# Kernel optimization log

Hardware: AMD Instinct MI355X
Metric: run time of the kernel (lower is better)

Reference implementation:

```python
import jax, jax.numpy as jnp
import numpy as np
import itertools

DIM, ORDER = 8, 4  # matches init_kwargs

def _exponent_table(dim, order):
    # All multisets (non-decreasing tuples) of size 0..order over range(dim),
    # sorted lexicographically -- identical to sorted(Counter keys) in the torch code
    # (Counter keys are sorted tuples; combinations_with_replacement yields exactly those).
    terms = sorted(itertools.chain.from_iterable(
        itertools.combinations_with_replacement(range(dim), o) for o in range(order + 1)))
    E = np.zeros((len(terms), dim), dtype=np.int32)
    for i, t in enumerate(terms):
        for d in t:
            E[i, d] += 1
    return E

E = jnp.asarray(_exponent_table(DIM, ORDER))  # [nterms=495, dim=8]


def setup_inputs() -> dict:
    key = jax.random.key(0)
    x = jax.random.normal(key, (65536, DIM), dtype=jnp.float32)
    return {"x": x}


def reference(x):
    # torch: cat_i prod_d x[..., d] ** ind_i.count(d)
    # vectorized: broadcast pow with exponent table, reduce-product over dim axis
    # x: [B, dim] -> [B, 1, dim] ** [nterms, dim] -> prod over dim -> [B, nterms]
    return jnp.prod(x[..., None, :] ** E, axis=-1)
```

## Files before the change

kernel.cpp:

```cpp
#include <hip/hip_runtime.h>


typedef float f32x4 __attribute__((ext_vector_type(4)));

struct Tbl {
    unsigned short e[64][8][4];
    unsigned short pp[64];
};

constexpr int pidx_c(int a, int b) {
    return 9 + 8 * a - (a * (a - 1)) / 2 + (b - a);
}

constexpr Tbl make_tbl() {
    Tbl T{};
    unsigned short lin[512] = {};
    int idx = 1;
    for (int a = 0; a < 8; ++a) {
        lin[idx++] = (unsigned short)(1 + a);
        for (int b = a; b < 8; ++b) {
            lin[idx++] = (unsigned short)pidx_c(a, b);
            for (int c = b; c < 8; ++c) {
                lin[idx++] = (unsigned short)(pidx_c(a, b) | ((1 + c) << 8));
                for (int d = c; d < 8; ++d)
                    lin[idx++] = (unsigned short)(pidx_c(a, b) | (pidx_c(c, d) << 8));
            }
        }
    }
    for (int l = 0; l < 64; ++l)
        for (int c = 0; c < 8; ++c)
            for (int k = 0; k < 4; ++k) {
                int ei = c * 256 + 4 * l + k;
                if (ei < 1980) {
                    int r = ei / 495, t = ei % 495;
                    int u = lin[t] & 255, v = lin[t] >> 8;
                    T.e[l][c][k] = (unsigned short)((r * 64 + u) | ((r * 64 + v) << 8));
                } else {
                    T.e[l][c][k] = 0;
                }
            }
    for (int l = 0; l < 64; ++l) {
        int s1 = 0, s2 = 0, u1 = 0, u2 = 0;
        if (l >= 1 && l <= 8) { s1 = l - 1; u1 = 1; }
        else if (l >= 9 && l < 45) {
            int k = l - 9, i = 0;
            while (k >= 8 - i) { k -= 8 - i; ++i; }
            s1 = i; s2 = i + k; u1 = 1; u2 = 1;
        }
        T.pp[l] = (unsigned short)(s1 | (s2 << 4) | (u1 << 8) | (u2 << 9));
    }
    return T;
}

__constant__ Tbl TBL = make_tbl();

#define WAVES_PER_BLOCK 4
#define ROWS_PER_WAVE   8
#define ROWS_PER_BLOCK  (WAVES_PER_BLOCK * ROWS_PER_WAVE)

__global__ __launch_bounds__(256, 8) void TotalDegree_29755533426739_kernel(
    const float* __restrict__ x, float* __restrict__ out, int B) {
    __shared__ float xs[ROWS_PER_BLOCK * 8];
    __shared__ float Pl[WAVES_PER_BLOCK][256];

    const int tid  = (int)threadIdx.x;
    const int lane = tid & 63;
    const int wid  = tid >> 6;

    {
        const int gi = (int)blockIdx.x * (ROWS_PER_BLOCK * 8) + tid;
        xs[tid] = (gi < B * 8) ? x[gi] : 0.0f;
    }

    const int ppv  = (int)TBL.pp[lane];
    const int s1   = ppv & 15;
    const int s2   = (ppv >> 4) & 15;
    const bool use1 = ((ppv >> 8) & 1) != 0;
    const bool use2 = ((ppv >> 9) & 1) != 0;

    unsigned long long tw[8];
    #pragma unroll
    for (int c = 0; c < 8; ++c)
        tw[c] = *reinterpret_cast<const unsigned long long*>(&TBL.e[lane][c][0]);

    __syncthreads();

    const float* xw = xs + wid * (ROWS_PER_WAVE * 8);
    float* Pw = Pl[wid];
    const unsigned rowBase =
        (unsigned)blockIdx.x * ROWS_PER_BLOCK + (unsigned)(wid * ROWS_PER_WAVE);

    #pragma unroll
    for (int g = 0; g < 2; ++g) {
        #pragma unroll
        for (int r = 0; r < 4; ++r) {
            const float a1 = xw[(g * 4 + r) * 8 + s1];
            const float a2 = xw[(g * 4 + r) * 8 + s2];
            Pw[r * 64 + lane] = (use1 ? a1 : 1.0f) * (use2 ? a2 : 1.0f);
        }

        float* o = out + (rowBase + (unsigned)(g * 4)) * 495u;
        f32x4* ob = reinterpret_cast<f32x4*>(o) + lane;

        #pragma unroll
        for (int c = 0; c < 8; ++c) {
            const unsigned w0 = (unsigned)tw[c];
            const unsigned w1 = (unsigned)(tw[c] >> 32);
            f32x4 v;
            v.x = Pw[w0 & 255] * Pw[(w0 >> 8) & 255];
            v.y = Pw[(w0 >> 16) & 255] * Pw[w0 >> 24];
            v.z = Pw[w1 & 255] * Pw[(w1 >> 8) & 255];
            v.w = Pw[(w1 >> 16) & 255] * Pw[w1 >> 24];
            if (c < 7) {
                ob[c * 64] = v;
            } else if (lane < 47) {
                ob[448] = v;
            }
        }
    }
}

extern "C" void kernel_launch(void* const* d_in, const int* in_sizes, int n_in,
                              void* d_out, int out_size, void* d_ws, size_t ws_size,
                              hipStream_t stream) {
    const float* x = (const float*)d_in[0];
    float* out = (float*)d_out;
    const int B = in_sizes[0] / 8;
    const int grid = (B + ROWS_PER_BLOCK - 1) / ROWS_PER_BLOCK;
    hipLaunchKernelGGL(TotalDegree_29755533426739_kernel,
                       dim3(grid), dim3(256), 0, stream, x, out, B);
}
```

Measured before the change: 145.8 us.

## Write block output as one contiguous stream with shared-memory term table

Instead of each wave writing its own 8 rows in 4-row groups, the block computes all 32 rows' degree-2 partial products into shared memory once. Its 4 waves then stream the block's contiguous 32x495 output region in 256-float units. The per-lane precomputed index words kept in registers are replaced by a per-term index table copied into LDS, and each lane locates its term and row by walking with fixed strides. This aims for fully contiguous, block-wide coalesced stores and fewer register-resident tables, at the cost of extra LDS lookups and index arithmetic per store.

```diff
diff --git a/kernel.cpp b/kernel.cpp
--- a/kernel.cpp
+++ b/kernel.cpp
@@ -4,7 +4,7 @@
 typedef float f32x4 __attribute__((ext_vector_type(4)));
 
 struct Tbl {
-    unsigned short e[64][8][4];
+    unsigned uv4[512];
     unsigned short pp[64];
 };
 
@@ -14,31 +14,21 @@
 
 constexpr Tbl make_tbl() {
     Tbl T{};
-    unsigned short lin[512] = {};
+    unsigned lin[500] = {};
     int idx = 1;
     for (int a = 0; a < 8; ++a) {
-        lin[idx++] = (unsigned short)(1 + a);
+        lin[idx++] = (unsigned)(1 + a);
         for (int b = a; b < 8; ++b) {
-            lin[idx++] = (unsigned short)pidx_c(a, b);
+            lin[idx++] = (unsigned)pidx_c(a, b);
             for (int c = b; c < 8; ++c) {
-                lin[idx++] = (unsigned short)(pidx_c(a, b) | ((1 + c) << 8));
+                lin[idx++] = (unsigned)pidx_c(a, b) | ((unsigned)(1 + c) << 16);
                 for (int d = c; d < 8; ++d)
-                    lin[idx++] = (unsigned short)(pidx_c(a, b) | (pidx_c(c, d) << 8));
+                    lin[idx++] = (unsigned)pidx_c(a, b) | ((unsigned)pidx_c(c, d) << 16);
             }
         }
     }
-    for (int l = 0; l < 64; ++l)
-        for (int c = 0; c < 8; ++c)
-            for (int k = 0; k < 4; ++k) {
-                int ei = c * 256 + 4 * l + k;
-                if (ei < 1980) {
-                    int r = ei / 495, t = ei % 495;
-                    int u = lin[t] & 255, v = lin[t] >> 8;
-                    T.e[l][c][k] = (unsigned short)((r * 64 + u) | ((r * 64 + v) << 8));
-                } else {
-                    T.e[l][c][k] = 0;
-                }
-            }
+    for (int i = 0; i < 5; ++i) lin[495 + i] = lin[i];
+    for (int t = 0; t < 499; ++t) T.uv4[(t & 3) * 128 + (t >> 2)] = lin[t];
     for (int l = 0; l < 64; ++l) {
         int s1 = 0, s2 = 0, u1 = 0, u2 = 0;
         if (l >= 1 && l <= 8) { s1 = l - 1; u1 = 1; }
@@ -54,21 +44,22 @@
 
 __constant__ Tbl TBL = make_tbl();
 
-#define WAVES_PER_BLOCK 4
-#define ROWS_PER_WAVE   8
-#define ROWS_PER_BLOCK  (WAVES_PER_BLOCK * ROWS_PER_WAVE)
+#define ROWS_PER_BLOCK 32
+#define WORDS_PER_BLOCK (ROWS_PER_BLOCK * 495)
+#define UNITS 62
 
 __global__ __launch_bounds__(256, 8) void TotalDegree_29755533426739_kernel(
     const float* __restrict__ x, float* __restrict__ out, int B) {
-    __shared__ float xs[ROWS_PER_BLOCK * 8];
-    __shared__ float Pl[WAVES_PER_BLOCK][256];
+    __shared__ float xs[256];
+    __shared__ float P[ROWS_PER_BLOCK * 64];
+    __shared__ unsigned uvt[512];
 
     const int tid  = (int)threadIdx.x;
     const int lane = tid & 63;
     const int wid  = tid >> 6;
 
     {
-        const int gi = (int)blockIdx.x * (ROWS_PER_BLOCK * 8) + tid;
+        const int gi = (int)blockIdx.x * 256 + tid;
         xs[tid] = (gi < B * 8) ? x[gi] : 0.0f;
     }
 
@@ -77,45 +68,43 @@
     const int s2   = (ppv >> 4) & 15;
     const bool use1 = ((ppv >> 8) & 1) != 0;
     const bool use2 = ((ppv >> 9) & 1) != 0;
-
-    unsigned long long tw[8];
+    const float* xw = xs + wid * 64;
     #pragma unroll
-    for (int c = 0; c < 8; ++c)
-        tw[c] = *reinterpret_cast<const unsigned long long*>(&TBL.e[lane][c][0]);
-
+    for (int rr = 0; rr < 8; ++rr) {
+        const float a1 = xw[rr * 8 + s1];
+        const float a2 = xw[rr * 8 + s2];
+        P[(wid * 8 + rr) * 64 + lane] = (use1 ? a1 : 1.0f) * (use2 ? a2 : 1.0f);
+    }
+    if (tid < 256) {
+        uvt[tid] = TBL.uv4[tid];
+        uvt[tid + 256] = TBL.uv4[tid + 256];
+    }
     __syncthreads();
 
-    const float* xw = xs + wid * (ROWS_PER_WAVE * 8);
-    float* Pw = Pl[wid];
-    const unsigned rowBase =
-        (unsigned)blockIdx.x * ROWS_PER_BLOCK + (unsigned)(wid * ROWS_PER_WAVE);
+    float* oB = out + (unsigned)blockIdx.x * WORDS_PER_BLOCK;
+    {
+        const int f0 = wid * 256 + (lane << 2);
+        int r0 = (f0 >= 990) ? 2 : (f0 >= 495 ? 1 : 0);
+        int t  = f0 - r0 * 495;
+        int rb = r0 << 6;
 
-    #pragma unroll
-    for (int g = 0; g < 2; ++g) {
-        #pragma unroll
-        for (int r = 0; r < 4; ++r) {
-            const float a1 = xw[(g * 4 + r) * 8 + s1];
-            const float a2 = xw[(g * 4 + r) * 8 + s2];
-            Pw[r * 64 + lane] = (use1 ? a1 : 1.0f) * (use2 ? a2 : 1.0f);
-        }
-
-        float* o = out + (rowBase + (unsigned)(g * 4)) * 495u;
-        f32x4* ob = reinterpret_cast<f32x4*>(o) + lane;
-
-        #pragma unroll
-        for (int c = 0; c < 8; ++c) {
-            const unsigned w0 = (unsigned)tw[c];
-            const unsigned w1 = (unsigned)(tw[c] >> 32);
+        for (int s = wid; s < UNITS; s += 4) {
+            const unsigned q0 = uvt[((t    ) & 3) * 128 + ((t    ) >> 2)];
+            const unsigned q1 = uvt[((t + 1) & 3) * 128 + ((t + 1) >> 2)];
+            const unsigned q2 = uvt[((t + 2) & 3) * 128 + ((t + 2) >> 2)];
+            const unsigned q3 = uvt[((t + 3) & 3) * 128 + ((t + 3) >> 2)];
+            const int w1 = (t >= 494) ? 64 : 0;
+            const int w2 = (t >= 493) ? 64 : 0;
+            const int w3 = (t >= 492) ? 64 : 0;
             f32x4 v;
-            v.x = Pw[w0 & 255] * Pw[(w0 >> 8) & 255];
-            v.y = Pw[(w0 >> 16) & 255] * Pw[w0 >> 24];
-            v.z = Pw[w1 & 255] * Pw[(w1 >> 8) & 255];
-            v.w = Pw[(w1 >> 16) & 255] * Pw[w1 >> 24];
-            if (c < 7) {
-                ob[c * 64] = v;
-            } else if (lane < 47) {
-                ob[448] = v;
-            }
+            v.x = P[rb      + (int)(q0 & 0xffffu)] * P[rb      + (int)(q0 >> 16)];
+            v.y = P[rb + w1 + (int)(q1 & 0xffffu)] * P[rb + w1 + (int)(q1 >> 16)];
+            v.z = P[rb + w2 + (int)(q2 & 0xffffu)] * P[rb + w2 + (int)(q2 >> 16)];
+            v.w = P[rb + w3 + (int)(q3 & 0xffffu)] * P[rb + w3 + (int)(q3 >> 16)];
+            if (s < UNITS - 1 || lane < 56)
+                *reinterpret_cast<f32x4*>(oB + s * 256 + (lane << 2)) = v;
+            t += 34; rb += 128;
+            if (t >= 495) { t -= 495; rb += 64; }
         }
     }
 }
```

After: 129.8 us. 11.0% less time.
